# Kernel tuning notes

Hardware: AMD Instinct MI355X
Metric: run time of the kernel (lower is better)

Reference implementation:

```python
import jax, jax.numpy as jnp
import numpy as np

THRESHOLD = 0.8
B, D, H, C = 8192, 4096, 8192, 2

def _mlp(x, w1, b1, w2, b2):
    h = jax.nn.relu(x @ w1 + b1)
    return h @ w2 + b2

def setup_inputs() -> dict:
    key = jax.random.key(0)
    ks = jax.random.split(key, 5)
    s1 = 1.0 / np.sqrt(D)
    s2 = 1.0 / np.sqrt(H)
    return {
        "x": jax.random.normal(ks[0], (B, D), dtype=jnp.float32),
        "t_w1": jax.random.normal(ks[1], (D, H), dtype=jnp.float32) * s1,
        "t_b1": jnp.zeros((H,), dtype=jnp.float32),
        "t_w2": jax.random.normal(ks[2], (H, C), dtype=jnp.float32) * s2,
        "t_b2": jnp.zeros((C,), dtype=jnp.float32),
        "f_w1": jax.random.normal(ks[3], (D, H), dtype=jnp.float32) * s1,
        "f_b1": jnp.zeros((H,), dtype=jnp.float32),
        "f_w2": jax.random.normal(ks[4], (H, C), dtype=jnp.float32) * s2,
        "f_b2": jnp.zeros((C,), dtype=jnp.float32),
    }

def reference(x, t_w1, t_b1, t_w2, t_b2, f_w1, f_b1, f_w2, f_b2):
    # Texture expert logits [B, C]
    t_out = _mlp(x, t_w1, t_b1, t_w2, t_b2)
    # Confidence = max softmax prob per row
    conf = jnp.max(jax.nn.softmax(t_out, axis=1), axis=1)
    low_conf = conf < THRESHOLD  # [B] bool
    # Frequency expert logits (jit-friendly: compute for all rows, select per row;
    # identical math to torch's masked gather/scatter)
    f_out = _mlp(x, f_w1, f_b1, f_w2, f_b2)
    return jnp.where(low_conf[:, None], f_out, t_out)
```

## Files before the change

kernel.cpp:

```cpp
#include <hip/hip_runtime.h>
#include <stdint.h>

typedef unsigned short u16;
typedef _Float16 f16x8 __attribute__((ext_vector_type(8)));
typedef float f32x4 __attribute__((ext_vector_type(4)));

#define B_ROWS 8192
#define K_DIM  4096
#define H_DIM  8192
#define W_SCALE 64.0f
#define INV_W_SCALE 0.015625f

__device__ __forceinline__ u16 f2h_bits(float f) {
  _Float16 h = (_Float16)f;
  return __builtin_bit_cast(u16, h);
}
__device__ __forceinline__ float h2f(u16 u) {
  return (float)__builtin_bit_cast(_Float16, u);
}

typedef __attribute__((address_space(1))) void gvoid_t;
typedef __attribute__((address_space(3))) void lvoid_t;
#define GLOAD_LDS16(gp, lp) \
  __builtin_amdgcn_global_load_lds((gvoid_t*)(gp), (lvoid_t*)(lp), 16, 0, 0)

__global__ void split_x_kernel(const float4* __restrict__ x,
                               ushort4* __restrict__ hi,
                               ushort4* __restrict__ lo, int n4) {
  int i = blockIdx.x * blockDim.x + threadIdx.x;
  if (i >= n4) return;
  float4 v = x[i];
  ushort4 h, l;
  h.x = f2h_bits(v.x); l.x = f2h_bits(v.x - h2f(h.x));
  h.y = f2h_bits(v.y); l.y = f2h_bits(v.y - h2f(h.y));
  h.z = f2h_bits(v.z); l.z = f2h_bits(v.z - h2f(h.z));
  h.w = f2h_bits(v.w); l.w = f2h_bits(v.w - h2f(h.w));
  hi[i] = h; lo[i] = l;
}

__global__ void transpose_split_kernel(const float* __restrict__ w,
                                       u16* __restrict__ hi, u16* __restrict__ lo,
                                       int rows, int cols) {
  __shared__ float tile[32][33];
  int c0 = blockIdx.x * 32, r0 = blockIdx.y * 32;
  int tx = threadIdx.x, ty = threadIdx.y;
  #pragma unroll
  for (int j = 0; j < 4; ++j)
    tile[ty + j*8][tx] = w[(size_t)(r0 + ty + j*8) * cols + c0 + tx];
  __syncthreads();
  #pragma unroll
  for (int j = 0; j < 4; ++j) {
    int oc = c0 + ty + j*8;
    float v = tile[tx][ty + j*8] * W_SCALE;
    u16 h = f2h_bits(v);
    size_t oidx = (size_t)oc * rows + r0 + tx;
    hi[oidx] = h;
    if (lo) lo[oidx] = f2h_bits(v - h2f(h));
  }
}

__global__ void init_parts_kernel(float* __restrict__ tp, float* __restrict__ fp,
                                  const float* __restrict__ tb2,
                                  const float* __restrict__ fb2) {
  int i = blockIdx.x * blockDim.x + threadIdx.x;
  if (i < 2 * B_ROWS) { tp[i] = tb2[i & 1]; fp[i] = fb2[i & 1]; }
}

__device__ __forceinline__ void epilogue(
    const f32x4 (&acc)[4][4], const float* __restrict__ b1,
    const float* __restrict__ w2, float* __restrict__ part,
    int bm, int bn, int wm, int wn, int q, int r)
{
  const int nbase = bn * 128 + wn * 64 + r;
  float b1v[4], w20[4], w21[4];
  #pragma unroll
  for (int t = 0; t < 4; ++t) {
    int n = nbase + t * 16;
    b1v[t] = b1[n];
    w20[t] = w2[2*n];
    w21[t] = w2[2*n + 1];
  }
  const int mbase = bm * 128 + wm * 64 + q * 4;
  #pragma unroll
  for (int tm = 0; tm < 4; ++tm) {
    #pragma unroll
    for (int v = 0; v < 4; ++v) {
      float s0 = 0.f, s1 = 0.f;
      #pragma unroll
      for (int tn = 0; tn < 4; ++tn) {
        float h = fmaxf(fmaf(acc[tm][tn][v], INV_W_SCALE, b1v[tn]), 0.f);
        s0 = fmaf(h, w20[tn], s0);
        s1 = fmaf(h, w21[tn], s1);
      }
      #pragma unroll
      for (int off = 1; off < 16; off <<= 1) {
        s0 += __shfl_xor(s0, off, 64);
        s1 += __shfl_xor(s1, off, 64);
      }
      if (r == 0) {
        int m = mbase + tm * 16 + v;
        atomicAdd(&part[2*m],     s0);
        atomicAdd(&part[2*m + 1], s1);
      }
    }
  }
}

__global__ __launch_bounds__(256, 2) void fused_mlp_kernel(
    const u16* __restrict__ xh, const u16* __restrict__ xl,
    const u16* __restrict__ twh, const u16* __restrict__ twl,
    const u16* __restrict__ fwh,
    const float* __restrict__ tb1, const float* __restrict__ tw2,
    const float* __restrict__ fb1, const float* __restrict__ fw2,
    float* __restrict__ tp, float* __restrict__ fp)
{
  __shared__ __align__(16) u16 lds[5 * 4096];

  const int tid  = threadIdx.x;
  const int lane = tid & 63;
  const int wave = tid >> 6;
  const int wm = wave >> 1;
  const int wn = wave & 1;
  const int q  = lane >> 4;
  const int r  = lane & 15;

  const int L  = blockIdx.x;
  const int s  = L >> 3;
  const int bm = s >> 3;
  const int bn = (L & 7) * 8 + (s & 7);

  unsigned aoff[2], boff[2];
  int ldsg[2];
  #pragma unroll
  for (int j = 0; j < 2; ++j) {
    int g = wave * 2 + j;
    int row_in = (g >> 2) * 64 + (g & 3) * 16 + r;
    aoff[j] = (unsigned)(bm * 128 + row_in) * K_DIM + q * 8;
    boff[j] = (unsigned)(bn * 128 + row_in) * K_DIM + q * 8;
    ldsg[j] = g * 512;
  }

  f32x4 at[4][4], af[4][4];
  #pragma unroll
  for (int i = 0; i < 4; ++i)
    #pragma unroll
    for (int j = 0; j < 4; ++j) {
      at[i][j] = (f32x4){0.f, 0.f, 0.f, 0.f};
      af[i][j] = (f32x4){0.f, 0.f, 0.f, 0.f};
    }

  for (int kk = 0; kk < K_DIM / 32; ++kk) {
    const unsigned ka = (unsigned)kk * 32u;
    __syncthreads();
    #pragma unroll
    for (int j = 0; j < 2; ++j) {
      GLOAD_LDS16(xh  + aoff[j] + ka, &lds[0*4096 + ldsg[j]]);
      GLOAD_LDS16(xl  + aoff[j] + ka, &lds[1*4096 + ldsg[j]]);
      GLOAD_LDS16(twh + boff[j] + ka, &lds[2*4096 + ldsg[j]]);
      GLOAD_LDS16(twl + boff[j] + ka, &lds[3*4096 + ldsg[j]]);
      GLOAD_LDS16(fwh + boff[j] + ka, &lds[4*4096 + ldsg[j]]);
    }
    __syncthreads();

    f16x8 ah[4], b0[4], tmp[4];
    #pragma unroll
    for (int t = 0; t < 4; ++t) {
      ah[t] = *reinterpret_cast<const f16x8*>(&lds[0*4096 + (wm*4 + t)*512 + lane*8]);
      b0[t] = *reinterpret_cast<const f16x8*>(&lds[2*4096 + (wn*4 + t)*512 + lane*8]);
    }
    #pragma unroll
    for (int tm = 0; tm < 4; ++tm)
      #pragma unroll
      for (int tn = 0; tn < 4; ++tn)
        at[tm][tn] = __builtin_amdgcn_mfma_f32_16x16x32_f16(ah[tm], b0[tn], at[tm][tn], 0, 0, 0);

    #pragma unroll
    for (int t = 0; t < 4; ++t)
      tmp[t] = *reinterpret_cast<const f16x8*>(&lds[1*4096 + (wm*4 + t)*512 + lane*8]);
    #pragma unroll
    for (int tm = 0; tm < 4; ++tm)
      #pragma unroll
      for (int tn = 0; tn < 4; ++tn)
        at[tm][tn] = __builtin_amdgcn_mfma_f32_16x16x32_f16(tmp[tm], b0[tn], at[tm][tn], 0, 0, 0);

    #pragma unroll
    for (int t = 0; t < 4; ++t)
      tmp[t] = *reinterpret_cast<const f16x8*>(&lds[3*4096 + (wn*4 + t)*512 + lane*8]);
    #pragma unroll
    for (int tm = 0; tm < 4; ++tm)
      #pragma unroll
      for (int tn = 0; tn < 4; ++tn)
        at[tm][tn] = __builtin_amdgcn_mfma_f32_16x16x32_f16(ah[tm], tmp[tn], at[tm][tn], 0, 0, 0);

    #pragma unroll
    for (int t = 0; t < 4; ++t)
      tmp[t] = *reinterpret_cast<const f16x8*>(&lds[4*4096 + (wn*4 + t)*512 + lane*8]);
    #pragma unroll
    for (int tm = 0; tm < 4; ++tm)
      #pragma unroll
      for (int tn = 0; tn < 4; ++tn)
        af[tm][tn] = __builtin_amdgcn_mfma_f32_16x16x32_f16(ah[tm], tmp[tn], af[tm][tn], 0, 0, 0);
  }

  epilogue(at, tb1, tw2, tp, bm, bn, wm, wn, q, r);
  epilogue(af, fb1, fw2, fp, bm, bn, wm, wn, q, r);
}

__global__ void select_kernel(const float* __restrict__ tp, const float* __restrict__ fp,
                              float* __restrict__ out) {
  int m = blockIdx.x * blockDim.x + threadIdx.x;
  if (m >= B_ROWS) return;
  float a = tp[2*m], b = tp[2*m + 1];
  float conf = 1.0f / (1.0f + expf(-fabsf(a - b)));
  bool low = conf < 0.8f;
  out[2*m]     = low ? fp[2*m]     : a;
  out[2*m + 1] = low ? fp[2*m + 1] : b;
}

extern "C" void kernel_launch(void* const* d_in, const int* in_sizes, int n_in,
                              void* d_out, int out_size, void* d_ws, size_t ws_size,
                              hipStream_t stream) {
  const float* x    = (const float*)d_in[0];
  const float* t_w1 = (const float*)d_in[1];
  const float* t_b1 = (const float*)d_in[2];
  const float* t_w2 = (const float*)d_in[3];
  const float* t_b2 = (const float*)d_in[4];
  const float* f_w1 = (const float*)d_in[5];
  const float* f_b1 = (const float*)d_in[6];
  const float* f_w2 = (const float*)d_in[7];
  const float* f_b2 = (const float*)d_in[8];
  float* out = (float*)d_out;

  const size_t SZ = (size_t)B_ROWS * K_DIM * sizeof(u16);
  const size_t NEED = 5 * SZ + 2 * (size_t)(2 * B_ROWS) * sizeof(float);
  if (ws_size < NEED) return;

  char* ws = (char*)d_ws;
  u16* x_hi   = (u16*)(ws);
  u16* x_lo   = (u16*)(ws + SZ);
  u16* twT_hi = (u16*)(ws + 2 * SZ);
  u16* twT_lo = (u16*)(ws + 3 * SZ);
  u16* fwT_hi = (u16*)(ws + 4 * SZ);
  float* t_part = (float*)(ws + 5 * SZ);
  float* f_part = t_part + 2 * B_ROWS;

  split_x_kernel<<<(B_ROWS * K_DIM / 4 + 255) / 256, 256, 0, stream>>>(
      (const float4*)x, (ushort4*)x_hi, (ushort4*)x_lo, B_ROWS * K_DIM / 4);
  dim3 tb(32, 8);
  transpose_split_kernel<<<dim3(H_DIM / 32, K_DIM / 32), tb, 0, stream>>>(
      t_w1, twT_hi, twT_lo, K_DIM, H_DIM);
  transpose_split_kernel<<<dim3(H_DIM / 32, K_DIM / 32), tb, 0, stream>>>(
      f_w1, fwT_hi, nullptr, K_DIM, H_DIM);
  init_parts_kernel<<<(2 * B_ROWS + 255) / 256, 256, 0, stream>>>(
      t_part, f_part, t_b2, f_b2);

  fused_mlp_kernel<<<(B_ROWS / 128) * (H_DIM / 128), 256, 0, stream>>>(
      x_hi, x_lo, twT_hi, twT_lo, fwT_hi,
      t_b1, t_w2, f_b1, f_w2, t_part, f_part);

  select_kernel<<<(B_ROWS + 255) / 256, 256, 0, stream>>>(t_part, f_part, out);
}
```

Measured before the change: 3.116 ms.

## Double-buffer LDS tiles and enlarge block to 256x128 with 512 threads

Replaces the load-sync-compute loop with a double-buffered LDS pipeline, so the global-to-LDS loads for the next K-step are issued before the current step's MFMAs. This removes one barrier per iteration and hides load latency. Blocks grow to 512 threads covering 256 rows by 128 columns, which halves how often each weight tile is re-read. All five workspace arrays are addressed from one base pointer plus a fixed stride. In exchange LDS use rises to about 112KB per block, which may cap occupancy below the two blocks requested by launch_bounds. The pointer scheme also relies on the workspace arrays being laid out contiguously at that exact stride.

Measured after the change: 2.868 ms. -8.0%, faster.

```diff
diff --git a/kernel.cpp b/kernel.cpp
--- a/kernel.cpp
+++ b/kernel.cpp
@@ -10,6 +10,8 @@
 #define H_DIM  8192
 #define W_SCALE 64.0f
 #define INV_W_SCALE 0.015625f
+
+#define ARR_STRIDE (33554432u)
 
 __device__ __forceinline__ u16 f2h_bits(float f) {
   _Float16 h = (_Float16)f;
@@ -69,9 +71,8 @@
 __device__ __forceinline__ void epilogue(
     const f32x4 (&acc)[4][4], const float* __restrict__ b1,
     const float* __restrict__ w2, float* __restrict__ part,
-    int bm, int bn, int wm, int wn, int q, int r)
+    int mbase, int nbase, int r)
 {
-  const int nbase = bn * 128 + wn * 64 + r;
   float b1v[4], w20[4], w21[4];
   #pragma unroll
   for (int t = 0; t < 4; ++t) {
@@ -80,7 +81,6 @@
     w20[t] = w2[2*n];
     w21[t] = w2[2*n + 1];
   }
-  const int mbase = bm * 128 + wm * 64 + q * 4;
   #pragma unroll
   for (int tm = 0; tm < 4; ++tm) {
     #pragma unroll
@@ -106,15 +106,14 @@
   }
 }
 
-__global__ __launch_bounds__(256, 2) void fused_mlp_kernel(
-    const u16* __restrict__ xh, const u16* __restrict__ xl,
-    const u16* __restrict__ twh, const u16* __restrict__ twl,
-    const u16* __restrict__ fwh,
+#define LBUF 28672
+__global__ __launch_bounds__(512, 2) void fused_mlp_kernel(
+    const u16* __restrict__ ws16,
     const float* __restrict__ tb1, const float* __restrict__ tw2,
     const float* __restrict__ fb1, const float* __restrict__ fw2,
     float* __restrict__ tp, float* __restrict__ fp)
 {
-  __shared__ __align__(16) u16 lds[5 * 4096];
+  __shared__ __align__(16) u16 lds[2 * LBUF];
 
   const int tid  = threadIdx.x;
   const int lane = tid & 63;
@@ -126,18 +125,23 @@
 
   const int L  = blockIdx.x;
   const int s  = L >> 3;
-  const int bm = s >> 3;
+  const int bm = (s >> 5) * 4 + ((s >> 3) & 3);
   const int bn = (L & 7) * 8 + (s & 7);
 
-  unsigned aoff[2], boff[2];
-  int ldsg[2];
-  #pragma unroll
-  for (int j = 0; j < 2; ++j) {
-    int g = wave * 2 + j;
-    int row_in = (g >> 2) * 64 + (g & 3) * 16 + r;
-    aoff[j] = (unsigned)(bm * 128 + row_in) * K_DIM + q * 8;
-    boff[j] = (unsigned)(bn * 128 + row_in) * K_DIM + q * 8;
-    ldsg[j] = g * 512;
+  unsigned goff[7];
+  int loff[7];
+  #pragma unroll
+  for (int j = 0; j < 7; ++j) {
+    int gid = wave * 7 + j;
+    unsigned arr; int g, lbase; bool isA;
+    if (gid < 16)      { arr = 0; g = gid;      lbase = 0;     isA = true;  }
+    else if (gid < 32) { arr = 1; g = gid - 16; lbase = 8192;  isA = true;  }
+    else if (gid < 40) { arr = 2; g = gid - 32; lbase = 16384; isA = false; }
+    else if (gid < 48) { arr = 3; g = gid - 40; lbase = 20480; isA = false; }
+    else               { arr = 4; g = gid - 48; lbase = 24576; isA = false; }
+    unsigned row = (isA ? (unsigned)bm * 256u : (unsigned)bn * 128u) + g * 16 + r;
+    goff[j] = arr * ARR_STRIDE + row * (unsigned)K_DIM + q * 8;
+    loff[j] = lbase + g * 512;
   }
 
   f32x4 at[4][4], af[4][4];
@@ -149,43 +153,47 @@
       af[i][j] = (f32x4){0.f, 0.f, 0.f, 0.f};
     }
 
+  #pragma unroll
+  for (int j = 0; j < 7; ++j)
+    GLOAD_LDS16(ws16 + goff[j], &lds[loff[j]]);
+
+  int p = 0;
   for (int kk = 0; kk < K_DIM / 32; ++kk) {
-    const unsigned ka = (unsigned)kk * 32u;
     __syncthreads();
-    #pragma unroll
-    for (int j = 0; j < 2; ++j) {
-      GLOAD_LDS16(xh  + aoff[j] + ka, &lds[0*4096 + ldsg[j]]);
-      GLOAD_LDS16(xl  + aoff[j] + ka, &lds[1*4096 + ldsg[j]]);
-      GLOAD_LDS16(twh + boff[j] + ka, &lds[2*4096 + ldsg[j]]);
-      GLOAD_LDS16(twl + boff[j] + ka, &lds[3*4096 + ldsg[j]]);
-      GLOAD_LDS16(fwh + boff[j] + ka, &lds[4*4096 + ldsg[j]]);
-    }
-    __syncthreads();
-
-    f16x8 ah[4], b0[4], tmp[4];
+
+    if (kk + 1 < K_DIM / 32) {
+      const unsigned ka = (unsigned)(kk + 1) * 32u;
+      const int lb = (p ^ 1) * LBUF;
+      #pragma unroll
+      for (int j = 0; j < 7; ++j)
+        GLOAD_LDS16(ws16 + goff[j] + ka, &lds[lb + loff[j]]);
+    }
+
+    const int base = p * LBUF;
+    f16x8 ah[4], bb[4], tmp[4];
     #pragma unroll
     for (int t = 0; t < 4; ++t) {
-      ah[t] = *reinterpret_cast<const f16x8*>(&lds[0*4096 + (wm*4 + t)*512 + lane*8]);
-      b0[t] = *reinterpret_cast<const f16x8*>(&lds[2*4096 + (wn*4 + t)*512 + lane*8]);
-    }
-    #pragma unroll
-    for (int tm = 0; tm < 4; ++tm)
-      #pragma unroll
-      for (int tn = 0; tn < 4; ++tn)
-        at[tm][tn] = __builtin_amdgcn_mfma_f32_16x16x32_f16(ah[tm], b0[tn], at[tm][tn], 0, 0, 0);
+      ah[t] = *reinterpret_cast<const f16x8*>(&lds[base + (wm*4 + t)*512 + lane*8]);
+      bb[t] = *reinterpret_cast<const f16x8*>(&lds[base + 16384 + (wn*4 + t)*512 + lane*8]);
+    }
+    #pragma unroll
+    for (int tm = 0; tm < 4; ++tm)
+      #pragma unroll
+      for (int tn = 0; tn < 4; ++tn)
+        at[tm][tn] = __builtin_amdgcn_mfma_f32_16x16x32_f16(ah[tm], bb[tn], at[tm][tn], 0, 0, 0);
 
     #pragma unroll
     for (int t = 0; t < 4; ++t)
-      tmp[t] = *reinterpret_cast<const f16x8*>(&lds[1*4096 + (wm*4 + t)*512 + lane*8]);
-    #pragma unroll
-    for (int tm = 0; tm < 4; ++tm)
-      #pragma unroll
-      for (int tn = 0; tn < 4; ++tn)
-        at[tm][tn] = __builtin_amdgcn_mfma_f32_16x16x32_f16(tmp[tm], b0[tn], at[tm][tn], 0, 0, 0);
+      tmp[t] = *reinterpret_cast<const f16x8*>(&lds[base + 8192 + (wm*4 + t)*512 + lane*8]);
+    #pragma unroll
+    for (int tm = 0; tm < 4; ++tm)
+      #pragma unroll
+      for (int tn = 0; tn < 4; ++tn)
+        at[tm][tn] = __builtin_amdgcn_mfma_f32_16x16x32_f16(tmp[tm], bb[tn], at[tm][tn], 0, 0, 0);
 
     #pragma unroll
     for (int t = 0; t < 4; ++t)
-      tmp[t] = *reinterpret_cast<const f16x8*>(&lds[3*4096 + (wn*4 + t)*512 + lane*8]);
+      tmp[t] = *reinterpret_cast<const f16x8*>(&lds[base + 20480 + (wn*4 + t)*512 + lane*8]);
     #pragma unroll
     for (int tm = 0; tm < 4; ++tm)
       #pragma unroll
@@ -194,16 +202,20 @@
 
     #pragma unroll
     for (int t = 0; t < 4; ++t)
-      tmp[t] = *reinterpret_cast<const f16x8*>(&lds[4*4096 + (wn*4 + t)*512 + lane*8]);
+      tmp[t] = *reinterpret_cast<const f16x8*>(&lds[base + 24576 + (wn*4 + t)*512 + lane*8]);
     #pragma unroll
     for (int tm = 0; tm < 4; ++tm)
       #pragma unroll
       for (int tn = 0; tn < 4; ++tn)
         af[tm][tn] = __builtin_amdgcn_mfma_f32_16x16x32_f16(ah[tm], tmp[tn], af[tm][tn], 0, 0, 0);
-  }
-
-  epilogue(at, tb1, tw2, tp, bm, bn, wm, wn, q, r);
-  epilogue(af, fb1, fw2, fp, bm, bn, wm, wn, q, r);
+
+    p ^= 1;
+  }
+
+  const int mbase = bm * 256 + wm * 64 + q * 4;
+  const int nbase = bn * 128 + wn * 64 + r;
+  epilogue(at, tb1, tw2, tp, mbase, nbase, r);
+  epilogue(af, fb1, fw2, fp, mbase, nbase, r);
 }
 
 __global__ void select_kernel(const float* __restrict__ tp, const float* __restrict__ fp,
@@ -254,9 +266,8 @@
   init_parts_kernel<<<(2 * B_ROWS + 255) / 256, 256, 0, stream>>>(
       t_part, f_part, t_b2, f_b2);
 
-  fused_mlp_kernel<<<(B_ROWS / 128) * (H_DIM / 128), 256, 0, stream>>>(
-      x_hi, x_lo, twT_hi, twT_lo, fwT_hi,
-      t_b1, t_w2, f_b1, f_w2, t_part, f_part);
+  fused_mlp_kernel<<<(B_ROWS / 256) * (H_DIM / 128), 512, 0, stream>>>(
+      x_hi, t_b1, t_w2, f_b1, f_w2, t_part, f_part);
 
   select_kernel<<<(B_ROWS + 255) / 256, 256, 0, stream>>>(t_part, f_part, out);
 }
```
